# Optimization experiments

Measured on AMD Instinct MI355X. Metric: run time of the kernel, lower is better.

The kernel has to match this reference:

```python
import jax, jax.numpy as jnp
import numpy as np

N_NODES = 100000
N_EDGES = 3200000
DIMS = [1, 64, 32, 16, 1]  # GCNConv channel sizes from __init__


def _add_self_loops(edge_index, n):
    loop = jnp.arange(n, dtype=edge_index.dtype)
    src = jnp.concatenate([edge_index[0], loop])
    dst = jnp.concatenate([edge_index[1], loop])
    return src, dst


def _deg_inv_sqrt(dst, n):
    # symmetric GCN norm: deg over destination nodes of A + I (edge_weight = 1)
    deg = jax.ops.segment_sum(jnp.ones_like(dst, dtype=jnp.float32), dst, num_segments=n)
    return jnp.where(deg > 0, jax.lax.rsqrt(deg), 0.0)


def _gcn_conv(x, src, dst, dinv, W, b, n):
    h = x @ W                                   # [N, out] transform first (PyG order)
    coef = dinv[src] * dinv[dst]                # [E+N] edge normalization
    out = jax.ops.segment_sum(coef[:, None] * h[src], dst, num_segments=n)
    return out + b


def setup_inputs() -> dict:
    key = jax.random.key(0)
    ks = jax.random.split(key, 12)
    x = jax.random.normal(ks[0], (N_NODES, DIMS[0]), dtype=jnp.float32)
    edge_index = jax.random.randint(ks[1], (2, N_EDGES), 0, N_NODES, dtype=jnp.int64)
    params = {}
    for i in range(4):
        fin, fout = DIMS[i], DIMS[i + 1]
        scale = 1.0 / np.sqrt(fin)
        params[f"W{i+1}"] = jax.random.uniform(ks[2 + 2 * i], (fin, fout), jnp.float32, -scale, scale)
        params[f"b{i+1}"] = jnp.zeros((fout,), jnp.float32)
    return {"x": x, "edge_index": edge_index, **params}


def reference(x, edge_index, W1, b1, W2, b2, W3, b3, W4, b4):
    n = x.shape[0]
    src, dst = _add_self_loops(edge_index, n)
    dinv = _deg_inv_sqrt(dst, n)
    h = jax.nn.relu(_gcn_conv(x, src, dst, dinv, W1, b1, n))
    h = jax.nn.relu(_gcn_conv(h, src, dst, dinv, W2, b2, n))
    h = jax.nn.relu(_gcn_conv(h, src, dst, dinv, W3, b3, n))
    h = _gcn_conv(h, src, dst, dinv, W4, b4, n)
    return h
```

## Files before the change

### kernel.cpp

```cpp
#include <hip/hip_runtime.h>

#define NPB_SHIFT 8
#define NPB 256
#define EPB 8192
#define MAXB 512
#define BCAP 9216
#define SRC_BITS 17
#define SRC_MASK 0x1FFFFu

__global__ void bcur_init_kernel(unsigned int* __restrict__ bcur, int NB) {
    int b = blockIdx.x * blockDim.x + threadIdx.x;
    if (b < NB) bcur[b] = (unsigned int)b * BCAP;
}

__global__ __launch_bounds__(256) void partition_kernel(const int* __restrict__ src,
                                                        const int* __restrict__ dst,
                                                        unsigned int* __restrict__ bcur,
                                                        unsigned int* __restrict__ staged, int E, int NB) {
    __shared__ unsigned int hist[MAXB], sc[MAXB], lbase[MAXB], lcur[MAXB], gbase[MAXB];
    __shared__ unsigned int stage[EPB];
    __shared__ unsigned short sbuck[EPB];
    int start = blockIdx.x * EPB;
    int cnt = min(EPB, E - start);
    for (int j = threadIdx.x; j < MAXB; j += 256) hist[j] = 0u;
    __syncthreads();
    for (int k = threadIdx.x; k < cnt; k += 256)
        atomicAdd(&hist[((unsigned int)dst[start + k]) >> NPB_SHIFT], 1u);
    __syncthreads();
    {
        int i0 = threadIdx.x, i1 = threadIdx.x + 256;
        sc[i0] = hist[i0]; sc[i1] = hist[i1];
        __syncthreads();
        for (int o = 1; o < MAXB; o <<= 1) {
            unsigned int v0 = (i0 >= o) ? sc[i0 - o] : 0u;
            unsigned int v1 = (i1 >= o) ? sc[i1 - o] : 0u;
            __syncthreads();
            sc[i0] += v0; sc[i1] += v1;
            __syncthreads();
        }
    }
    for (int j = threadIdx.x; j < MAXB; j += 256) {
        unsigned int c = hist[j];
        unsigned int ex = sc[j] - c;
        lbase[j] = ex; lcur[j] = ex;
        gbase[j] = (j < NB && c) ? atomicAdd(&bcur[j], c) : 0u;
    }
    __syncthreads();
    for (int k = threadIdx.x; k < cnt; k += 256) {
        unsigned int d = (unsigned int)dst[start + k];
        unsigned int b = d >> NPB_SHIFT;
        unsigned int pos = atomicAdd(&lcur[b], 1u);
        stage[pos] = ((d & (NPB - 1)) << SRC_BITS) | (unsigned int)src[start + k];
        sbuck[pos] = (unsigned short)b;
    }
    __syncthreads();
    for (int t = threadIdx.x; t < cnt; t += 256) {
        unsigned int b = sbuck[t];
        staged[(size_t)gbase[b] + (t - lbase[b])] = stage[t];
    }
}

__global__ __launch_bounds__(256) void build_csr_kernel(const unsigned int* __restrict__ staged,
                                                        const unsigned int* __restrict__ bcur,
                                                        const float* __restrict__ x,
                                                        unsigned int* __restrict__ csr,
                                                        unsigned int* __restrict__ off,
                                                        unsigned int* __restrict__ deg,
                                                        float* __restrict__ dinv,
                                                        float* __restrict__ ttx, int N) {
    __shared__ unsigned int cnt[NPB], loff[NPB], ncur[NPB];
    int b = blockIdx.x;
    unsigned int base = (unsigned int)b * BCAP;
    unsigned int m = bcur[b] - base;
    int node0 = b << NPB_SHIFT;
    cnt[threadIdx.x] = 0u;
    __syncthreads();
    for (unsigned int t = threadIdx.x; t < m; t += 256)
        atomicAdd(&cnt[staged[(size_t)base + t] >> SRC_BITS], 1u);
    __syncthreads();
    unsigned int v = cnt[threadIdx.x];
    loff[threadIdx.x] = v;
    __syncthreads();
    for (int o = 1; o < NPB; o <<= 1) {
        unsigned int a = (threadIdx.x >= (unsigned)o) ? loff[threadIdx.x - o] : 0u;
        __syncthreads();
        loff[threadIdx.x] += a;
        __syncthreads();
    }
    unsigned int ex = loff[threadIdx.x] - v;
    ncur[threadIdx.x] = ex;
    int node = node0 + threadIdx.x;
    if (node < N) {
        off[node] = base + ex;
        deg[node] = v;
        float di = 1.0f / sqrtf((float)(v + 1u));
        dinv[node] = di;
        ttx[node] = di * x[node];
    }
    __syncthreads();
    for (unsigned int t = threadIdx.x; t < m; t += 256) {
        unsigned int rec = staged[(size_t)base + t];
        unsigned int p = atomicAdd(&ncur[rec >> SRC_BITS], 1u);
        csr[(size_t)base + p] = rec & SRC_MASK;
    }
}

__global__ __launch_bounds__(256) void lut_kernel(const float* __restrict__ W1, const float* __restrict__ b1,
                                                  const float* __restrict__ W2,
                                                  float* __restrict__ Alut, float* __restrict__ Blut,
                                                  float* __restrict__ tvals) {
    __shared__ float w1[64], bb[64], tv[64];
    __shared__ int rnk[64];
    __shared__ float sW2[64 * 32];
    __shared__ double red[2][256];
    int tid = threadIdx.x;
    if (tid < 64) {
        float w = W1[tid], b = b1[tid];
        w1[tid] = w; bb[tid] = b;
        tv[tid] = (w != 0.f) ? (-b / w) : __uint_as_float(0x7F800000u);
    }
    for (int t = tid; t < 64 * 32; t += 256) sW2[t] = W2[t];
    __syncthreads();
    if (tid < 64) {
        int r = 0;
        float tj = tv[tid];
        for (int k = 0; k < 64; ++k)
            if (w1[k] != 0.f && (tv[k] < tj || (tv[k] == tj && k < tid))) ++r;
        rnk[tid] = r;
        if (blockIdx.x == 0) tvals[tid] = tv[tid];
    }
    __syncthreads();
    int s = blockIdx.x;
    int c = tid & 31, slice = tid >> 5;
    double da = 0.0, db = 0.0;
#pragma unroll
    for (int u = 0; u < 8; ++u) {
        int j = slice * 8 + u;
        float w = w1[j];
        bool act = (w > 0.f) ? (rnk[j] < s) : ((w < 0.f) ? (rnk[j] >= s) : (bb[j] > 0.f));
        if (act) {
            double w2 = (double)sW2[j * 32 + c];
            da += (double)w * w2;
            db += (double)bb[j] * w2;
        }
    }
    red[0][tid] = da; red[1][tid] = db;
    __syncthreads();
    for (int o = 128; o >= 32; o >>= 1) {
        if (tid < o) { red[0][tid] += red[0][tid + o]; red[1][tid] += red[1][tid + o]; }
        __syncthreads();
    }
    if (tid < 32) {
        Alut[s * 32 + tid] = (float)red[0][tid];
        Blut[s * 32 + tid] = (float)red[1][tid];
    }
}

__global__ __launch_bounds__(256) void gather1_kernel(const unsigned int* __restrict__ csr,
                                                      const unsigned int* __restrict__ off,
                                                      const unsigned int* __restrict__ deg,
                                                      const float* __restrict__ dinv,
                                                      const float* __restrict__ tt,
                                                      const float* __restrict__ tvals,
                                                      uint4* __restrict__ recs, int N) {
    __shared__ float st[64];
    for (int t = threadIdx.x; t < 64; t += 256) st[t] = tvals[t];
    __syncthreads();
    int tid = blockIdx.x * 256 + threadIdx.x;
    int i = tid >> 2, l = tid & 3;
    if (i >= N) return;
    unsigned int o = off[i], n = deg[i];
    float acc0 = 0.f, acc1 = 0.f;
    unsigned int k = l;
    for (; k + 4 < n; k += 8) { acc0 += tt[csr[o + k]]; acc1 += tt[csr[o + k + 4]]; }
    if (k < n) acc0 += tt[csr[o + k]];
    float acc = acc0 + acc1;
    acc += __shfl_xor(acc, 1, 4);
    acc += __shfl_xor(acc, 2, 4);
    float di = dinv[i];
    float a = di * (acc + tt[i]);
    unsigned int cv = 0;
#pragma unroll
    for (int j = 0; j < 16; ++j) cv += (st[l * 16 + j] < a) ? 1u : 0u;
    cv += __shfl_xor(cv, 1, 4);
    cv += __shfl_xor(cv, 2, 4);
    if (l == 0) recs[i] = make_uint4(__float_as_uint(a * di), __float_as_uint(di), cv, 0u);
}

#define G2_NODES 64
__global__ __launch_bounds__(256) void gather2t3_kernel(const unsigned int* __restrict__ csr,
                                                        const unsigned int* __restrict__ off,
                                                        const unsigned int* __restrict__ deg,
                                                        const float* __restrict__ dinv,
                                                        const uint4* __restrict__ recs,
                                                        const float* __restrict__ Alut, const float* __restrict__ Blut,
                                                        const float* __restrict__ b2, const float* __restrict__ W3,
                                                        float* __restrict__ tt3, int N) {
    __shared__ float4 sAB[65 * 16];
    __shared__ float sW3[32 * 16];
    __shared__ float sb2[32];
    for (int t = threadIdx.x; t < 65 * 16; t += 256) {
        int s = t >> 4, cc = t & 15;
        sAB[t] = make_float4(Alut[s * 32 + cc], Alut[s * 32 + cc + 16],
                             Blut[s * 32 + cc], Blut[s * 32 + cc + 16]);
    }
    for (int t = threadIdx.x; t < 32 * 16; t += 256) sW3[t] = W3[t];
    if (threadIdx.x < 32) sb2[threadIdx.x] = b2[threadIdx.x];
    __syncthreads();

    int g = threadIdx.x >> 4, c = threadIdx.x & 15;
    for (int iter = 0; iter < 4; ++iter) {
        int d = blockIdx.x * G2_NODES + iter * 16 + g;
        if (d >= N) continue;
        float dd = dinv[d];
        unsigned int o = off[d], n = deg[d];
        uint4 rs = recs[d];
        float ps = __uint_as_float(rs.x), qs = __uint_as_float(rs.y);
        float4 ABs = sAB[rs.z * 16 + c];
        float2 a0 = make_float2(fmaf(ABs.x, ps, ABs.z * qs), fmaf(ABs.y, ps, ABs.w * qs));
        float2 a1 = make_float2(0.f, 0.f), a2 = make_float2(0.f, 0.f), a3 = make_float2(0.f, 0.f);
        unsigned int k = 0;
        for (; k + 3 < n; k += 4) {
            unsigned int s0 = csr[o + k], s1 = csr[o + k + 1], s2 = csr[o + k + 2], s3 = csr[o + k + 3];
            uint4 r0 = recs[s0], r1 = recs[s1], r2 = recs[s2], r3 = recs[s3];
            float4 A0 = sAB[r0.z * 16 + c], A1 = sAB[r1.z * 16 + c];
            float4 A2 = sAB[r2.z * 16 + c], A3 = sAB[r3.z * 16 + c];
            float p0 = __uint_as_float(r0.x), q0 = __uint_as_float(r0.y);
            float p1 = __uint_as_float(r1.x), q1 = __uint_as_float(r1.y);
            float p2 = __uint_as_float(r2.x), q2 = __uint_as_float(r2.y);
            float p3 = __uint_as_float(r3.x), q3 = __uint_as_float(r3.y);
            a0.x = fmaf(A0.x, p0, fmaf(A0.z, q0, a0.x));
            a0.y = fmaf(A0.y, p0, fmaf(A0.w, q0, a0.y));
            a1.x = fmaf(A1.x, p1, fmaf(A1.z, q1, a1.x));
            a1.y = fmaf(A1.y, p1, fmaf(A1.w, q1, a1.y));
            a2.x = fmaf(A2.x, p2, fmaf(A2.z, q2, a2.x));
            a2.y = fmaf(A2.y, p2, fmaf(A2.w, q2, a2.y));
            a3.x = fmaf(A3.x, p3, fmaf(A3.z, q3, a3.x));
            a3.y = fmaf(A3.y, p3, fmaf(A3.w, q3, a3.y));
        }
        for (; k < n; ++k) {
            unsigned int s0 = csr[o + k];
            uint4 r0 = recs[s0];
            float4 A0 = sAB[r0.z * 16 + c];
            float p0 = __uint_as_float(r0.x), q0 = __uint_as_float(r0.y);
            a0.x = fmaf(A0.x, p0, fmaf(A0.z, q0, a0.x));
            a0.y = fmaf(A0.y, p0, fmaf(A0.w, q0, a0.y));
        }
        float hx = fmaxf(fmaf(dd, (a0.x + a1.x) + (a2.x + a3.x), sb2[c]), 0.f);
        float hy = fmaxf(fmaf(dd, (a0.y + a1.y) + (a2.y + a3.y), sb2[c + 16]), 0.f);

        float t3 = 0.f;
#pragma unroll
        for (int kk = 0; kk < 16; ++kk) {
            float hk = __shfl(hx, kk, 16);
            t3 = fmaf(hk, sW3[kk * 16 + c], t3);
        }
#pragma unroll
        for (int kk = 0; kk < 16; ++kk) {
            float hk = __shfl(hy, kk, 16);
            t3 = fmaf(hk, sW3[(kk + 16) * 16 + c], t3);
        }
        tt3[(size_t)d * 16 + c] = dd * t3;
    }
}

__global__ __launch_bounds__(256) void gather3t4_kernel(const unsigned int* __restrict__ csr,
                                                        const unsigned int* __restrict__ off,
                                                        const unsigned int* __restrict__ deg,
                                                        const float* __restrict__ dinv,
                                                        const float* __restrict__ tt3,
                                                        const float* __restrict__ b3, const float* __restrict__ W4,
                                                        float* __restrict__ tt4, int N) {
    int tid = blockIdx.x * 256 + threadIdx.x;
    int d = tid >> 2, l = tid & 3;
    if (d >= N) return;
    float dd = dinv[d];
    unsigned int o = off[d], n = deg[d];
    const float4* t34 = reinterpret_cast<const float4*>(tt3);
    float4 acc = t34[(size_t)d * 4 + l];
    float4 acc1 = make_float4(0.f, 0.f, 0.f, 0.f);
    unsigned int k = 0;
    for (; k + 3 < n; k += 4) {
        unsigned int s0 = csr[o + k], s1 = csr[o + k + 1], s2 = csr[o + k + 2], s3 = csr[o + k + 3];
        float4 v0 = t34[(size_t)s0 * 4 + l];
        float4 v1 = t34[(size_t)s1 * 4 + l];
        float4 v2 = t34[(size_t)s2 * 4 + l];
        float4 v3 = t34[(size_t)s3 * 4 + l];
        acc.x += v0.x + v2.x; acc.y += v0.y + v2.y; acc.z += v0.z + v2.z; acc.w += v0.w + v2.w;
        acc1.x += v1.x + v3.x; acc1.y += v1.y + v3.y; acc1.z += v1.z + v3.z; acc1.w += v1.w + v3.w;
    }
    for (; k < n; ++k) {
        float4 v0 = t34[(size_t)csr[o + k] * 4 + l];
        acc.x += v0.x; acc.y += v0.y; acc.z += v0.z; acc.w += v0.w;
    }
    acc.x += acc1.x; acc.y += acc1.y; acc.z += acc1.z; acc.w += acc1.w;
    float4 b3v = reinterpret_cast<const float4*>(b3)[l];
    float4 w4v = reinterpret_cast<const float4*>(W4)[l];
    float v = fmaxf(fmaf(dd, acc.x, b3v.x), 0.f) * w4v.x;
    v = fmaf(fmaxf(fmaf(dd, acc.y, b3v.y), 0.f), w4v.y, v);
    v = fmaf(fmaxf(fmaf(dd, acc.z, b3v.z), 0.f), w4v.z, v);
    v = fmaf(fmaxf(fmaf(dd, acc.w, b3v.w), 0.f), w4v.w, v);
    v += __shfl_xor(v, 1, 4);
    v += __shfl_xor(v, 2, 4);
    if (l == 0) tt4[d] = dd * v;
}

__global__ void gather4_kernel(const unsigned int* __restrict__ csr, const unsigned int* __restrict__ off,
                               const unsigned int* __restrict__ deg, const float* __restrict__ dinv,
                               const float* __restrict__ tt, const float* __restrict__ b4,
                               float* __restrict__ out, int N) {
    int tid = blockIdx.x * blockDim.x + threadIdx.x;
    int i = tid >> 2, l = tid & 3;
    if (i >= N) return;
    unsigned int o = off[i], n = deg[i];
    float acc0 = 0.f, acc1 = 0.f;
    unsigned int k = l;
    for (; k + 4 < n; k += 8) { acc0 += tt[csr[o + k]]; acc1 += tt[csr[o + k + 4]]; }
    if (k < n) acc0 += tt[csr[o + k]];
    float acc = acc0 + acc1;
    acc += __shfl_xor(acc, 1, 4);
    acc += __shfl_xor(acc, 2, 4);
    if (l == 0) out[i] = dinv[i] * (acc + tt[i]) + b4[0];
}

extern "C" void kernel_launch(void* const* d_in, const int* in_sizes, int n_in,
                              void* d_out, int out_size, void* d_ws, size_t ws_size,
                              hipStream_t stream) {
    const float* x  = (const float*)d_in[0];
    const int* eidx = (const int*)d_in[1];
    const float* W1 = (const float*)d_in[2];
    const float* b1 = (const float*)d_in[3];
    const float* W2 = (const float*)d_in[4];
    const float* b2 = (const float*)d_in[5];
    const float* W3 = (const float*)d_in[6];
    const float* b3 = (const float*)d_in[7];
    const float* W4 = (const float*)d_in[8];
    const float* b4 = (const float*)d_in[9];
    float* out = (float*)d_out;

    const int N = in_sizes[0];
    const int E = in_sizes[1] / 2;
    const int* src = eidx;
    const int* dst = eidx + E;
    const int NB = (N + NPB - 1) >> NPB_SHIFT;

    char* ws = (char*)d_ws;
    unsigned int* bcur  = (unsigned int*)ws;  ws += MAXB * 4;
    float* tvals = (float*)ws;                ws += 64 * 4;
    float* Alut  = (float*)ws;                ws += 65 * 32 * 4;
    float* Blut  = (float*)ws;                ws += 65 * 32 * 4;
    unsigned int* off = (unsigned int*)ws;    ws += (size_t)N * 4;
    unsigned int* deg = (unsigned int*)ws;    ws += (size_t)N * 4;
    float* dinv = (float*)ws;                 ws += (size_t)N * 4;
    float* ttx  = (float*)ws;                 ws += (size_t)N * 4;
    float* tt4  = (float*)ws;                 ws += (size_t)N * 4;
    uint4* recs = (uint4*)ws;                 ws += (size_t)N * 16;
    unsigned int* csr = (unsigned int*)ws;    ws += (size_t)NB * BCAP * 4;
    unsigned int* staged = (unsigned int*)ws;
    float* tt3 = (float*)staged;

    const int nPartBlocks = (E + EPB - 1) / EPB;

    bcur_init_kernel<<<(NB + 255) / 256, 256, 0, stream>>>(bcur, NB);
    partition_kernel<<<nPartBlocks, 256, 0, stream>>>(src, dst, bcur, staged, E, NB);
    build_csr_kernel<<<NB, 256, 0, stream>>>(staged, bcur, x, csr, off, deg, dinv, ttx, N);
    lut_kernel<<<65, 256, 0, stream>>>(W1, b1, W2, Alut, Blut, tvals);

    gather1_kernel<<<((size_t)N * 4 + 255) / 256, 256, 0, stream>>>(csr, off, deg, dinv, ttx, tvals, recs, N);
    gather2t3_kernel<<<(N + G2_NODES - 1) / G2_NODES, 256, 0, stream>>>(csr, off, deg, dinv, recs, Alut, Blut, b2, W3, tt3, N);
    gather3t4_kernel<<<((size_t)N * 4 + 255) / 256, 256, 0, stream>>>(csr, off, deg, dinv, tt3, b3, W4, tt4, N);
    gather4_kernel<<<((size_t)N * 4 + 255) / 256, 256, 0, stream>>>(csr, off, deg, dinv, tt4, b4, out, N);
}
```

Before: 218.9 us.

## Pre-expand neighbor records into edge order for sequential layer-2 gather

Adds an expand kernel that writes each edge's 16-byte source-node record into an edge-ordered array, so the layer-2 gather reads records contiguously instead of through an indirect random gather. The new path is used only when the workspace is large enough for the extra array of roughly NB*BCAP*16 bytes. The fallback gather's unroll is also cut from 4 to 2. The trade is an extra pass that still does the random gather once and writes about 50MB, in return for coalesced reads where 16 lanes share each record load.

```diff
diff --git a/kernel.cpp b/kernel.cpp
--- a/kernel.cpp
+++ b/kernel.cpp
@@ -5,6 +5,7 @@
 #define EPB 8192
 #define MAXB 512
 #define BCAP 9216
+#define BPB 36
 #define SRC_BITS 17
 #define SRC_MASK 0x1FFFFu
 
@@ -187,7 +188,91 @@
     if (l == 0) recs[i] = make_uint4(__float_as_uint(a * di), __float_as_uint(di), cv, 0u);
 }
 
+__global__ __launch_bounds__(256) void expand_kernel(const unsigned int* __restrict__ csr,
+                                                     const unsigned int* __restrict__ bcur,
+                                                     const uint4* __restrict__ recs,
+                                                     uint4* __restrict__ erecs) {
+    int b = blockIdx.x / BPB;
+    unsigned int slot = (unsigned int)b * BCAP + (unsigned int)(blockIdx.x % BPB) * 256 + threadIdx.x;
+    if (slot < bcur[b]) erecs[slot] = recs[csr[slot]];
+}
+
 #define G2_NODES 64
+__global__ __launch_bounds__(256) void gather2t3_seq_kernel(const uint4* __restrict__ erecs,
+                                                            const unsigned int* __restrict__ off,
+                                                            const unsigned int* __restrict__ deg,
+                                                            const float* __restrict__ dinv,
+                                                            const uint4* __restrict__ recs,
+                                                            const float* __restrict__ Alut, const float* __restrict__ Blut,
+                                                            const float* __restrict__ b2, const float* __restrict__ W3,
+                                                            float* __restrict__ tt3, int N) {
+    __shared__ float4 sAB[65 * 16];
+    __shared__ float sW3[32 * 16];
+    __shared__ float sb2[32];
+    for (int t = threadIdx.x; t < 65 * 16; t += 256) {
+        int s = t >> 4, cc = t & 15;
+        sAB[t] = make_float4(Alut[s * 32 + cc], Alut[s * 32 + cc + 16],
+                             Blut[s * 32 + cc], Blut[s * 32 + cc + 16]);
+    }
+    for (int t = threadIdx.x; t < 32 * 16; t += 256) sW3[t] = W3[t];
+    if (threadIdx.x < 32) sb2[threadIdx.x] = b2[threadIdx.x];
+    __syncthreads();
+
+    int g = threadIdx.x >> 4, c = threadIdx.x & 15;
+    for (int iter = 0; iter < 4; ++iter) {
+        int d = blockIdx.x * G2_NODES + iter * 16 + g;
+        if (d >= N) continue;
+        float dd = dinv[d];
+        unsigned int o = off[d], n = deg[d];
+        uint4 rs = recs[d];
+        float ps = __uint_as_float(rs.x), qs = __uint_as_float(rs.y);
+        float4 ABs = sAB[rs.z * 16 + c];
+        float2 a0 = make_float2(fmaf(ABs.x, ps, ABs.z * qs), fmaf(ABs.y, ps, ABs.w * qs));
+        float2 a1 = make_float2(0.f, 0.f), a2 = make_float2(0.f, 0.f), a3 = make_float2(0.f, 0.f);
+        const uint4* ep = erecs + o;
+        unsigned int k = 0;
+        for (; k + 3 < n; k += 4) {
+            uint4 r0 = ep[k], r1 = ep[k + 1], r2 = ep[k + 2], r3 = ep[k + 3];
+            float4 A0 = sAB[r0.z * 16 + c], A1 = sAB[r1.z * 16 + c];
+            float4 A2 = sAB[r2.z * 16 + c], A3 = sAB[r3.z * 16 + c];
+            float p0 = __uint_as_float(r0.x), q0 = __uint_as_float(r0.y);
+            float p1 = __uint_as_float(r1.x), q1 = __uint_as_float(r1.y);
+            float p2 = __uint_as_float(r2.x), q2 = __uint_as_float(r2.y);
+            float p3 = __uint_as_float(r3.x), q3 = __uint_as_float(r3.y);
+            a0.x = fmaf(A0.x, p0, fmaf(A0.z, q0, a0.x));
+            a0.y = fmaf(A0.y, p0, fmaf(A0.w, q0, a0.y));
+            a1.x = fmaf(A1.x, p1, fmaf(A1.z, q1, a1.x));
+            a1.y = fmaf(A1.y, p1, fmaf(A1.w, q1, a1.y));
+            a2.x = fmaf(A2.x, p2, fmaf(A2.z, q2, a2.x));
+            a2.y = fmaf(A2.y, p2, fmaf(A2.w, q2, a2.y));
+            a3.x = fmaf(A3.x, p3, fmaf(A3.z, q3, a3.x));
+            a3.y = fmaf(A3.y, p3, fmaf(A3.w, q3, a3.y));
+        }
+        for (; k < n; ++k) {
+            uint4 r0 = ep[k];
+            float4 A0 = sAB[r0.z * 16 + c];
+            float p0 = __uint_as_float(r0.x), q0 = __uint_as_float(r0.y);
+            a0.x = fmaf(A0.x, p0, fmaf(A0.z, q0, a0.x));
+            a0.y = fmaf(A0.y, p0, fmaf(A0.w, q0, a0.y));
+        }
+        float hx = fmaxf(fmaf(dd, (a0.x + a1.x) + (a2.x + a3.x), sb2[c]), 0.f);
+        float hy = fmaxf(fmaf(dd, (a0.y + a1.y) + (a2.y + a3.y), sb2[c + 16]), 0.f);
+
+        float t3 = 0.f;
+#pragma unroll
+        for (int kk = 0; kk < 16; ++kk) {
+            float hk = __shfl(hx, kk, 16);
+            t3 = fmaf(hk, sW3[kk * 16 + c], t3);
+        }
+#pragma unroll
+        for (int kk = 0; kk < 16; ++kk) {
+            float hk = __shfl(hy, kk, 16);
+            t3 = fmaf(hk, sW3[(kk + 16) * 16 + c], t3);
+        }
+        tt3[(size_t)d * 16 + c] = dd * t3;
+    }
+}
+
 __global__ __launch_bounds__(256) void gather2t3_kernel(const unsigned int* __restrict__ csr,
                                                         const unsigned int* __restrict__ off,
                                                         const unsigned int* __restrict__ deg,
@@ -207,7 +292,6 @@
     for (int t = threadIdx.x; t < 32 * 16; t += 256) sW3[t] = W3[t];
     if (threadIdx.x < 32) sb2[threadIdx.x] = b2[threadIdx.x];
     __syncthreads();
-
     int g = threadIdx.x >> 4, c = threadIdx.x & 15;
     for (int iter = 0; iter < 4; ++iter) {
         int d = blockIdx.x * G2_NODES + iter * 16 + g;
@@ -218,27 +302,20 @@
         float ps = __uint_as_float(rs.x), qs = __uint_as_float(rs.y);
         float4 ABs = sAB[rs.z * 16 + c];
         float2 a0 = make_float2(fmaf(ABs.x, ps, ABs.z * qs), fmaf(ABs.y, ps, ABs.w * qs));
-        float2 a1 = make_float2(0.f, 0.f), a2 = make_float2(0.f, 0.f), a3 = make_float2(0.f, 0.f);
+        float2 a1 = make_float2(0.f, 0.f);
         unsigned int k = 0;
-        for (; k + 3 < n; k += 4) {
-            unsigned int s0 = csr[o + k], s1 = csr[o + k + 1], s2 = csr[o + k + 2], s3 = csr[o + k + 3];
-            uint4 r0 = recs[s0], r1 = recs[s1], r2 = recs[s2], r3 = recs[s3];
+        for (; k + 1 < n; k += 2) {
+            unsigned int s0 = csr[o + k], s1 = csr[o + k + 1];
+            uint4 r0 = recs[s0], r1 = recs[s1];
             float4 A0 = sAB[r0.z * 16 + c], A1 = sAB[r1.z * 16 + c];
-            float4 A2 = sAB[r2.z * 16 + c], A3 = sAB[r3.z * 16 + c];
             float p0 = __uint_as_float(r0.x), q0 = __uint_as_float(r0.y);
             float p1 = __uint_as_float(r1.x), q1 = __uint_as_float(r1.y);
-            float p2 = __uint_as_float(r2.x), q2 = __uint_as_float(r2.y);
-            float p3 = __uint_as_float(r3.x), q3 = __uint_as_float(r3.y);
             a0.x = fmaf(A0.x, p0, fmaf(A0.z, q0, a0.x));
             a0.y = fmaf(A0.y, p0, fmaf(A0.w, q0, a0.y));
             a1.x = fmaf(A1.x, p1, fmaf(A1.z, q1, a1.x));
             a1.y = fmaf(A1.y, p1, fmaf(A1.w, q1, a1.y));
-            a2.x = fmaf(A2.x, p2, fmaf(A2.z, q2, a2.x));
-            a2.y = fmaf(A2.y, p2, fmaf(A2.w, q2, a2.y));
-            a3.x = fmaf(A3.x, p3, fmaf(A3.z, q3, a3.x));
-            a3.y = fmaf(A3.y, p3, fmaf(A3.w, q3, a3.y));
-        }
-        for (; k < n; ++k) {
+        }
+        if (k < n) {
             unsigned int s0 = csr[o + k];
             uint4 r0 = recs[s0];
             float4 A0 = sAB[r0.z * 16 + c];
@@ -246,9 +323,8 @@
             a0.x = fmaf(A0.x, p0, fmaf(A0.z, q0, a0.x));
             a0.y = fmaf(A0.y, p0, fmaf(A0.w, q0, a0.y));
         }
-        float hx = fmaxf(fmaf(dd, (a0.x + a1.x) + (a2.x + a3.x), sb2[c]), 0.f);
-        float hy = fmaxf(fmaf(dd, (a0.y + a1.y) + (a2.y + a3.y), sb2[c + 16]), 0.f);
-
+        float hx = fmaxf(fmaf(dd, a0.x + a1.x, sb2[c]), 0.f);
+        float hy = fmaxf(fmaf(dd, a0.y + a1.y, sb2[c + 16]), 0.f);
         float t3 = 0.f;
 #pragma unroll
         for (int kk = 0; kk < 16; ++kk) {
@@ -345,6 +421,7 @@
     const int NB = (N + NPB - 1) >> NPB_SHIFT;
 
     char* ws = (char*)d_ws;
+    char* ws0 = ws;
     unsigned int* bcur  = (unsigned int*)ws;  ws += MAXB * 4;
     float* tvals = (float*)ws;                ws += 64 * 4;
     float* Alut  = (float*)ws;                ws += 65 * 32 * 4;
@@ -356,8 +433,11 @@
     float* tt4  = (float*)ws;                 ws += (size_t)N * 4;
     uint4* recs = (uint4*)ws;                 ws += (size_t)N * 16;
     unsigned int* csr = (unsigned int*)ws;    ws += (size_t)NB * BCAP * 4;
-    unsigned int* staged = (unsigned int*)ws;
+    unsigned int* staged = (unsigned int*)ws; ws += (size_t)NB * BCAP * 4;
     float* tt3 = (float*)staged;
+    uint4* erecs = (uint4*)ws;
+    size_t need_erecs = (size_t)(ws - ws0) + (size_t)NB * BCAP * 16;
+    const bool use_expand = (ws_size >= need_erecs);
 
     const int nPartBlocks = (E + EPB - 1) / EPB;
 
@@ -367,7 +447,12 @@
     lut_kernel<<<65, 256, 0, stream>>>(W1, b1, W2, Alut, Blut, tvals);
 
     gather1_kernel<<<((size_t)N * 4 + 255) / 256, 256, 0, stream>>>(csr, off, deg, dinv, ttx, tvals, recs, N);
-    gather2t3_kernel<<<(N + G2_NODES - 1) / G2_NODES, 256, 0, stream>>>(csr, off, deg, dinv, recs, Alut, Blut, b2, W3, tt3, N);
+    if (use_expand) {
+        expand_kernel<<<NB * BPB, 256, 0, stream>>>(csr, bcur, recs, erecs);
+        gather2t3_seq_kernel<<<(N + G2_NODES - 1) / G2_NODES, 256, 0, stream>>>(erecs, off, deg, dinv, recs, Alut, Blut, b2, W3, tt3, N);
+    } else {
+        gather2t3_kernel<<<(N + G2_NODES - 1) / G2_NODES, 256, 0, stream>>>(csr, off, deg, dinv, recs, Alut, Blut, b2, W3, tt3, N);
+    }
     gather3t4_kernel<<<((size_t)N * 4 + 255) / 256, 256, 0, stream>>>(csr, off, deg, dinv, tt3, b3, W4, tt4, N);
     gather4_kernel<<<((size_t)N * 4 + 255) / 256, 256, 0, stream>>>(csr, off, deg, dinv, tt4, b4, out, N);
 }
```

New measurement: 227.9 us. 4.1% more time.
